# Optimization experiments

Measured on AMD Instinct MI355X. Metric: run time of the kernel, lower is better.

Reference implementation:

```python
import jax, jax.numpy as jnp
import numpy as np

B, T, U = 32, 512, 64
V, H, E = 32000, 512, 512


def setup_inputs() -> dict:
    key = jax.random.key(0)
    ks = jax.random.split(key, 12)
    s = 0.02
    return {
        "encoder_out": jax.random.normal(ks[0], (B, T, E), jnp.float32),
        "encoder_lens": jax.random.randint(ks[1], (B,), 1, T + 1),
        "decoder_in": jax.random.randint(ks[2], (B, U), 0, V),
        "emb_table": jax.random.normal(ks[3], (V, H), jnp.float32) * s,
        "W_attn": jax.random.normal(ks[4], (H, E), jnp.float32) * s,
        "W_ih0": jax.random.normal(ks[5], (3 * H, H + E), jnp.float32) * s,
        "W_hh0": jax.random.normal(ks[6], (3 * H, H), jnp.float32) * s,
        "b_ih0": jnp.zeros((3 * H,), jnp.float32),
        "b_hh0": jnp.zeros((3 * H,), jnp.float32),
        "W_ih1": jax.random.normal(ks[7], (3 * H, H), jnp.float32) * s,
        "W_hh1": jax.random.normal(ks[8], (3 * H, H), jnp.float32) * s,
        "b_ih1": jnp.zeros((3 * H,), jnp.float32),
        "b_hh1": jnp.zeros((3 * H,), jnp.float32),
        "W_out": jax.random.normal(ks[9], (V, H + E), jnp.float32) * s,
        "b_out": jnp.zeros((V,), jnp.float32),
    }


def gru_cell(x, h, W_ih, W_hh, b_ih, b_hh):
    # PyTorch GRUCell gate math
    gi = x @ W_ih.T + b_ih          # [B, 3H]
    gh = h @ W_hh.T + b_hh          # [B, 3H]
    i_r, i_z, i_n = jnp.split(gi, 3, axis=-1)
    h_r, h_z, h_n = jnp.split(gh, 3, axis=-1)
    r = jax.nn.sigmoid(i_r + h_r)
    z = jax.nn.sigmoid(i_z + h_z)
    n = jnp.tanh(i_n + r * h_n)
    return (1.0 - z) * n + z * h


def reference(encoder_out, encoder_lens, decoder_in, emb_table, W_attn,
              W_ih0, W_hh0, b_ih0, b_hh0, W_ih1, W_hh1, b_ih1, b_hh1,
              W_out, b_out):
    b, t_max, e = encoder_out.shape
    u_max = decoder_in.shape[1]
    enc_proj = jnp.einsum('bte,he->bth', encoder_out, W_attn)   # [B,T,H]
    embedded = emb_table[decoder_in]                            # [B,U,H]
    pad_mask = jnp.arange(t_max)[None, :] >= encoder_lens[:, None]  # [B,T]
    h_dim = emb_table.shape[1]

    def step(carry, xs):
        h0, h1 = carry
        emb_t, t = xs                                           # emb_t: [B,H]
        # first step: query is the embedding; afterwards: top-layer hidden
        query = jnp.where(t == 0, emb_t, h1)
        scores = jnp.einsum('bth,bh->bt', enc_proj, query)      # [B,T]
        scores = jnp.where(pad_mask, -jnp.inf, scores)
        attn = jax.nn.softmax(scores, axis=1)
        context = jnp.einsum('bt,bte->be', attn, encoder_out)   # [B,E]
        x = jnp.concatenate([emb_t, context], axis=-1)          # [B,H+E]
        h0n = gru_cell(x, h0, W_ih0, W_hh0, b_ih0, b_hh0)
        h1n = gru_cell(h0n, h1, W_ih1, W_hh1, b_ih1, b_hh1)     # dropout=eval mode (no-op)
        logits = jnp.concatenate([h1n, context], axis=-1) @ W_out.T + b_out  # [B,V]
        return (h0n, h1n), logits

    init = (jnp.zeros((b, h_dim), encoder_out.dtype),
            jnp.zeros((b, h_dim), encoder_out.dtype))
    xs = (jnp.swapaxes(embedded, 0, 1), jnp.arange(u_max))
    _, logits = jax.lax.scan(step, init, xs)                    # [U,B,V]
    return jnp.swapaxes(logits, 0, 1)                           # [B,U,V]
```

## Files before the change

kernel.cpp:

```cpp
#include <hip/hip_runtime.h>
#include <math.h>

#define B_ 32
#define T_ 512
#define U_ 64
#define V_ 32000
#define H_ 512
#define E_ 512

typedef short short8 __attribute__((ext_vector_type(8)));
typedef float f32x4 __attribute__((ext_vector_type(4)));

__global__ void embed_kernel(const int* __restrict__ tok, const float* __restrict__ table,
                             float* __restrict__ out) {
  int row = blockIdx.x;
  int t = tok[row];
  const float4* src = (const float4*)(table + (size_t)t * H_);
  float4* dst = (float4*)(out + (size_t)row * H_);
  dst[threadIdx.x] = src[threadIdx.x];
}

__global__ void zero_kernel(float* p, int n) {
  int i = blockIdx.x * blockDim.x + threadIdx.x;
  if (i < n) p[i] = 0.f;
}

__device__ __forceinline__ unsigned pack1(float f) {
  unsigned u = __float_as_uint(f);
  unsigned hi = u & 0xffff0000u;
  float lo = f - __uint_as_float(hi);
  return hi | (__float_as_uint(lo) >> 16);
}

__global__ __launch_bounds__(256) void pack_kernel(const float4* __restrict__ src,
                                                   uint4* __restrict__ dst, int n4) {
  int i = blockIdx.x * blockDim.x + threadIdx.x;
  if (i < n4) {
    float4 f = src[i];
    uint4 o;
    o.x = pack1(f.x); o.y = pack1(f.y); o.z = pack1(f.z); o.w = pack1(f.w);
    dst[i] = o;
  }
}

__global__ __launch_bounds__(256) void gemm_abt(
    const float* __restrict__ A, const float* __restrict__ Bm,
    const float* __restrict__ bias, float* __restrict__ C,
    int N, int K, int lda, int ldb) {
  __shared__ float As[8][128];
  __shared__ float Bs[8][128];
  int tid = threadIdx.x;
  int n0 = blockIdx.x * 128, m0 = blockIdx.y * 128;
  int lr = tid >> 1;
  int lk = (tid & 1) * 4;
  const float* Ap = A + (size_t)(m0 + lr) * lda + lk;
  const float* Bp = Bm + (size_t)(n0 + lr) * ldb + lk;
  int tx = tid & 15, ty = tid >> 4;
  float acc[8][8];
#pragma unroll
  for (int i = 0; i < 8; i++)
#pragma unroll
    for (int j = 0; j < 8; j++) acc[i][j] = 0.f;

  for (int k0 = 0; k0 < K; k0 += 8) {
    float4 av = *(const float4*)(Ap + k0);
    float4 bv = *(const float4*)(Bp + k0);
    __syncthreads();
    As[lk + 0][lr] = av.x; As[lk + 1][lr] = av.y; As[lk + 2][lr] = av.z; As[lk + 3][lr] = av.w;
    Bs[lk + 0][lr] = bv.x; Bs[lk + 1][lr] = bv.y; Bs[lk + 2][lr] = bv.z; Bs[lk + 3][lr] = bv.w;
    __syncthreads();
#pragma unroll
    for (int kk = 0; kk < 8; kk++) {
      float a[8], b[8];
      *(float4*)&a[0] = *(const float4*)&As[kk][ty * 4];
      *(float4*)&a[4] = *(const float4*)&As[kk][ty * 4 + 64];
      *(float4*)&b[0] = *(const float4*)&Bs[kk][tx * 4];
      *(float4*)&b[4] = *(const float4*)&Bs[kk][tx * 4 + 64];
#pragma unroll
      for (int i = 0; i < 8; i++)
#pragma unroll
        for (int j = 0; j < 8; j++) acc[i][j] = fmaf(a[i], b[j], acc[i][j]);
    }
  }
  float bb[8] = {0, 0, 0, 0, 0, 0, 0, 0};
  if (bias) {
    *(float4*)&bb[0] = *(const float4*)&bias[n0 + tx * 4];
    *(float4*)&bb[4] = *(const float4*)&bias[n0 + tx * 4 + 64];
  }
#pragma unroll
  for (int i = 0; i < 8; i++) {
    int m = m0 + ty * 4 + (i & 3) + (i >> 2) * 64;
    float* Crow = C + (size_t)m * N + n0;
    float4 o0 = make_float4(acc[i][0] + bb[0], acc[i][1] + bb[1], acc[i][2] + bb[2], acc[i][3] + bb[3]);
    float4 o1 = make_float4(acc[i][4] + bb[4], acc[i][5] + bb[5], acc[i][6] + bb[6], acc[i][7] + bb[7]);
    *(float4*)(Crow + tx * 4) = o0;
    *(float4*)(Crow + tx * 4 + 64) = o1;
  }
}

__device__ __forceinline__ void unpack8(uint4 u0, uint4 u1, short8& h, short8& l) {
  h[0] = (short)(u0.x >> 16); l[0] = (short)(u0.x & 0xffffu);
  h[1] = (short)(u0.y >> 16); l[1] = (short)(u0.y & 0xffffu);
  h[2] = (short)(u0.z >> 16); l[2] = (short)(u0.z & 0xffffu);
  h[3] = (short)(u0.w >> 16); l[3] = (short)(u0.w & 0xffffu);
  h[4] = (short)(u1.x >> 16); l[4] = (short)(u1.x & 0xffffu);
  h[5] = (short)(u1.y >> 16); l[5] = (short)(u1.y & 0xffffu);
  h[6] = (short)(u1.z >> 16); l[6] = (short)(u1.z & 0xffffu);
  h[7] = (short)(u1.w >> 16); l[7] = (short)(u1.w & 0xffffu);
}

__global__ __launch_bounds__(256) void gemm_mfma(
    const unsigned* __restrict__ Ap, const unsigned* __restrict__ Bp,
    const float* __restrict__ bias, float* __restrict__ C, int N, int K) {
  __shared__ __align__(16) unsigned As[128 * 64];
  __shared__ __align__(16) unsigned Bs[128 * 64];
  int tid = threadIdx.x;
  int n0 = blockIdx.x * 128, m0 = blockIdx.y * 128;
  int w = tid >> 6, l = tid & 63;
  int wm = (w >> 1) * 64, wn = (w & 1) * 64;
  f32x4 acc[4][4];
#pragma unroll
  for (int i = 0; i < 4; i++)
#pragma unroll
    for (int j = 0; j < 4; j++) acc[i][j] = (f32x4){0.f, 0.f, 0.f, 0.f};

  for (int kt = 0; kt < K; kt += 64) {
    __syncthreads();
#pragma unroll
    for (int i = 0; i < 8; i++) {
      int off16 = tid + i * 256;
      int row = off16 >> 4, c = off16 & 15;
      int sc = c ^ (row & 15);
      *(uint4*)&As[(size_t)off16 * 4] = *(const uint4*)&Ap[(size_t)(m0 + row) * K + kt + sc * 4];
      *(uint4*)&Bs[(size_t)off16 * 4] = *(const uint4*)&Bp[(size_t)(n0 + row) * K + kt + sc * 4];
    }
    __syncthreads();
#pragma unroll
    for (int kk = 0; kk < 2; kk++) {
      short8 ah[4], al[4], bh[4], bl[4];
      int c0 = kk * 8 + (l >> 4) * 2;
#pragma unroll
      for (int fm = 0; fm < 4; fm++) {
        int row = wm + fm * 16 + (l & 15);
        uint4 u0 = *(const uint4*)&As[(row * 16 + (c0 ^ (row & 15))) * 4];
        uint4 u1 = *(const uint4*)&As[(row * 16 + ((c0 + 1) ^ (row & 15))) * 4];
        unpack8(u0, u1, ah[fm], al[fm]);
      }
#pragma unroll
      for (int fn = 0; fn < 4; fn++) {
        int row = wn + fn * 16 + (l & 15);
        uint4 u0 = *(const uint4*)&Bs[(row * 16 + (c0 ^ (row & 15))) * 4];
        uint4 u1 = *(const uint4*)&Bs[(row * 16 + ((c0 + 1) ^ (row & 15))) * 4];
        unpack8(u0, u1, bh[fn], bl[fn]);
      }
#pragma unroll
      for (int fm = 0; fm < 4; fm++)
#pragma unroll
        for (int fn = 0; fn < 4; fn++) {
          acc[fm][fn] = __builtin_amdgcn_mfma_f32_16x16x32_bf16(ah[fm], bh[fn], acc[fm][fn], 0, 0, 0);
          acc[fm][fn] = __builtin_amdgcn_mfma_f32_16x16x32_bf16(ah[fm], bl[fn], acc[fm][fn], 0, 0, 0);
          acc[fm][fn] = __builtin_amdgcn_mfma_f32_16x16x32_bf16(al[fm], bh[fn], acc[fm][fn], 0, 0, 0);
        }
    }
  }
#pragma unroll
  for (int fn = 0; fn < 4; fn++) {
    int n = n0 + wn + fn * 16 + (l & 15);
    float bz = bias ? bias[n] : 0.f;
#pragma unroll
    for (int fm = 0; fm < 4; fm++) {
      int mbase = m0 + wm + fm * 16 + (l >> 4) * 4;
#pragma unroll
      for (int r = 0; r < 4; r++) C[(size_t)(mbase + r) * N + n] = acc[fm][fn][r] + bz;
    }
  }
}

__global__ __launch_bounds__(512) void attn_scores(
    const float* __restrict__ enc_proj, const int* __restrict__ lens,
    const float* __restrict__ embedded, const float* __restrict__ h1_prev,
    float* __restrict__ sc_raw, int u) {
  int s = blockIdx.x, b = blockIdx.y;
  int tid = threadIdx.x;
  __shared__ __align__(16) float q[H_];
  q[tid] = (u == 0) ? embedded[((size_t)b * U_ + u) * H_ + tid] : h1_prev[b * H_ + tid];
  __syncthreads();
  int len = lens[b];
  int w = tid >> 6, l = tid & 63;
  int t0 = s * 64 + w * 8;
  const float4* q4 = (const float4*)q;
  float4 b0 = q4[l], b1 = q4[l + 64];
#pragma unroll
  for (int i = 0; i < 8; i++) {
    int t = t0 + i;
    if (t < len) {
      const float4* r4 = (const float4*)(enc_proj + ((size_t)b * T_ + t) * H_);
      float4 a0 = r4[l], a1 = r4[l + 64];
      float acc = a0.x * b0.x + a0.y * b0.y + a0.z * b0.z + a0.w * b0.w
                + a1.x * b1.x + a1.y * b1.y + a1.z * b1.z + a1.w * b1.w;
#pragma unroll
      for (int off = 32; off > 0; off >>= 1) acc += __shfl_xor(acc, off, 64);
      if (l == 0) sc_raw[b * T_ + t] = acc;
    } else {
      if (l == 0) sc_raw[b * T_ + t] = -INFINITY;
    }
  }
}

__global__ __launch_bounds__(512) void attn_ctx(
    const float* __restrict__ enc_out, const float* __restrict__ sc_raw,
    float* __restrict__ X, int u) {
  int s = blockIdx.x, b = blockIdx.y;
  int tid = threadIdx.x;
  __shared__ float p[T_];
  __shared__ float red[512];
  float v = sc_raw[b * T_ + tid];
  red[tid] = v;
  __syncthreads();
  for (int st = 256; st > 0; st >>= 1) { if (tid < st) red[tid] = fmaxf(red[tid], red[tid + st]); __syncthreads(); }
  float mx = red[0];
  __syncthreads();
  float e = expf(v - mx);
  red[tid] = e;
  __syncthreads();
  for (int st = 256; st > 0; st >>= 1) { if (tid < st) red[tid] += red[tid + st]; __syncthreads(); }
  float inv = 1.f / red[0];
  __syncthreads();
  p[tid] = e * inv;
  __syncthreads();
  int l = tid & 63, stripe = tid >> 6;
  const float* eo = enc_out + (size_t)b * T_ * E_ + s * 64 + l;
  float a0 = 0, a1 = 0, a2 = 0, a3 = 0, a4 = 0, a5 = 0, a6 = 0, a7 = 0;
  for (int t = stripe; t < T_; t += 64) {
    a0 += p[t]      * eo[(size_t)(t)      * E_];
    a1 += p[t +  8] * eo[(size_t)(t +  8) * E_];
    a2 += p[t + 16] * eo[(size_t)(t + 16) * E_];
    a3 += p[t + 24] * eo[(size_t)(t + 24) * E_];
    a4 += p[t + 32] * eo[(size_t)(t + 32) * E_];
    a5 += p[t + 40] * eo[(size_t)(t + 40) * E_];
    a6 += p[t + 48] * eo[(size_t)(t + 48) * E_];
    a7 += p[t + 56] * eo[(size_t)(t + 56) * E_];
  }
  red[tid] = a0 + a1 + a2 + a3 + a4 + a5 + a6 + a7;
  __syncthreads();
  if (tid < 64) {
    float r = red[tid];
#pragma unroll
    for (int i = 1; i < 8; i++) r += red[tid + 64 * i];
    X[((size_t)b * U_ + u) * (H_ + E_) + H_ + s * 64 + tid] = r;
  }
}

__global__ __launch_bounds__(256) void gru0_step(
    const float* __restrict__ X, const float* __restrict__ GI0,
    const float* __restrict__ h_prev, const float* __restrict__ W_ih,
    const float* __restrict__ W_hh, const float* __restrict__ b_ih,
    const float* __restrict__ b_hh, float* __restrict__ h_next, int u) {
  int j = blockIdx.x;
  int tid = threadIdx.x;
  __shared__ __align__(16) float Wr[512], Wz[512], Wn[512], Vr[512], Vz[512], Vn[512];
  __shared__ float red[4][256];
  {
    int h2 = tid & 127;
    const float4* wr4 = (const float4*)(W_ih + (size_t)j * 1024 + 512);
    const float4* wz4 = (const float4*)(W_ih + ((size_t)j + 512) * 1024 + 512);
    const float4* wn4 = (const float4*)(W_ih + ((size_t)j + 1024) * 1024 + 512);
    const float4* vr4 = (const float4*)(W_hh + (size_t)j * 512);
    const float4* vz4 = (const float4*)(W_hh + ((size_t)j + 512) * 512);
    const float4* vn4 = (const float4*)(W_hh + ((size_t)j + 1024) * 512);
    if (tid < 128) {
      ((float4*)Wr)[h2] = wr4[h2];
      ((float4*)Wn)[h2] = wn4[h2];
      ((float4*)Vz)[h2] = vz4[h2];
    } else {
      ((float4*)Wz)[h2] = wz4[h2];
      ((float4*)Vr)[h2] = vr4[h2];
      ((float4*)Vn)[h2] = vn4[h2];
    }
  }
  __syncthreads();
  int b = tid >> 3, s = tid & 7;
  const float4* xc = (const float4*)(X + ((size_t)b * U_ + u) * (H_ + E_) + H_);
  const float4* hp = (const float4*)(h_prev + (size_t)b * H_);
  float ar = 0, az = 0, ain = 0, ahn = 0;
#pragma unroll 4
  for (int i = 0; i < 16; i++) {
    int k4 = s + i * 8;
    float4 xv = xc[k4];
    float4 hv = hp[k4];
    float4 wr = ((const float4*)Wr)[k4];
    float4 wz = ((const float4*)Wz)[k4];
    float4 wn = ((const float4*)Wn)[k4];
    float4 vr = ((const float4*)Vr)[k4];
    float4 vz = ((const float4*)Vz)[k4];
    float4 vn = ((const float4*)Vn)[k4];
    ar += wr.x * xv.x + wr.y * xv.y + wr.z * xv.z + wr.w * xv.w
        + vr.x * hv.x + vr.y * hv.y + vr.z * hv.z + vr.w * hv.w;
    az += wz.x * xv.x + wz.y * xv.y + wz.z * xv.z + wz.w * xv.w
        + vz.x * hv.x + vz.y * hv.y + vz.z * hv.z + vz.w * hv.w;
    ain += wn.x * xv.x + wn.y * xv.y + wn.z * xv.z + wn.w * xv.w;
    ahn += vn.x * hv.x + vn.y * hv.y + vn.z * hv.z + vn.w * hv.w;
  }
  red[0][tid] = ar; red[1][tid] = az; red[2][tid] = ain; red[3][tid] = ahn;
  __syncthreads();
  if (tid < 32) {
    int bb = tid;
    float r = 0, z = 0, in_ = 0, hn = 0;
#pragma unroll
    for (int q2 = 0; q2 < 8; q2++) {
      r += red[0][bb * 8 + q2]; z += red[1][bb * 8 + q2];
      in_ += red[2][bb * 8 + q2]; hn += red[3][bb * 8 + q2];
    }
    size_t grow = ((size_t)bb * U_ + u) * 1536;
    r += GI0[grow + j] + b_ih[j] + b_hh[j];
    z += GI0[grow + 512 + j] + b_ih[512 + j] + b_hh[512 + j];
    in_ += GI0[grow + 1024 + j];
    float rg = 1.f / (1.f + expf(-r));
    float zg = 1.f / (1.f + expf(-z));
    float n = tanhf(in_ + b_ih[1024 + j] + rg * (hn + b_hh[1024 + j]));
    h_next[bb * H_ + j] = (1.f - zg) * n + zg * h_prev[bb * H_ + j];
  }
}

__global__ __launch_bounds__(256) void gru1_step(
    const float* __restrict__ xin, const float* __restrict__ h_prev,
    const float* __restrict__ W_ih, const float* __restrict__ W_hh,
    const float* __restrict__ b_ih, const float* __restrict__ b_hh,
    float* __restrict__ h_next, float* __restrict__ X, int u) {
  int j = blockIdx.x;
  int tid = threadIdx.x;
  __shared__ __align__(16) float Wr[512], Wz[512], Wn[512], Vr[512], Vz[512], Vn[512];
  __shared__ float red[4][256];
  {
    int h2 = tid & 127;
    const float4* wr4 = (const float4*)(W_ih + (size_t)j * 512);
    const float4* wz4 = (const float4*)(W_ih + ((size_t)j + 512) * 512);
    const float4* wn4 = (const float4*)(W_ih + ((size_t)j + 1024) * 512);
    const float4* vr4 = (const float4*)(W_hh + (size_t)j * 512);
    const float4* vz4 = (const float4*)(W_hh + ((size_t)j + 512) * 512);
    const float4* vn4 = (const float4*)(W_hh + ((size_t)j + 1024) * 512);
    if (tid < 128) {
      ((float4*)Wr)[h2] = wr4[h2];
      ((float4*)Wn)[h2] = wn4[h2];
      ((float4*)Vz)[h2] = vz4[h2];
    } else {
      ((float4*)Wz)[h2] = wz4[h2];
      ((float4*)Vr)[h2] = vr4[h2];
      ((float4*)Vn)[h2] = vn4[h2];
    }
  }
  __syncthreads();
  int b = tid >> 3, s = tid & 7;
  const float4* xp = (const float4*)(xin + (size_t)b * H_);
  const float4* hp = (const float4*)(h_prev + (size_t)b * H_);
  float ar = 0, az = 0, ain = 0, ahn = 0;
#pragma unroll 4
  for (int i = 0; i < 16; i++) {
    int k4 = s + i * 8;
    float4 xv = xp[k4];
    float4 hv = hp[k4];
    float4 wr = ((const float4*)Wr)[k4];
    float4 wz = ((const float4*)Wz)[k4];
    float4 wn = ((const float4*)Wn)[k4];
    float4 vr = ((const float4*)Vr)[k4];
    float4 vz = ((const float4*)Vz)[k4];
    float4 vn = ((const float4*)Vn)[k4];
    ar += wr.x * xv.x + wr.y * xv.y + wr.z * xv.z + wr.w * xv.w
        + vr.x * hv.x + vr.y * hv.y + vr.z * hv.z + vr.w * hv.w;
    az += wz.x * xv.x + wz.y * xv.y + wz.z * xv.z + wz.w * xv.w
        + vz.x * hv.x + vz.y * hv.y + vz.z * hv.z + vz.w * hv.w;
    ain += wn.x * xv.x + wn.y * xv.y + wn.z * xv.z + wn.w * xv.w;
    ahn += vn.x * hv.x + vn.y * hv.y + vn.z * hv.z + vn.w * hv.w;
  }
  red[0][tid] = ar; red[1][tid] = az; red[2][tid] = ain; red[3][tid] = ahn;
  __syncthreads();
  if (tid < 32) {
    int bb = tid;
    float r = 0, z = 0, in_ = 0, hn = 0;
#pragma unroll
    for (int q2 = 0; q2 < 8; q2++) {
      r += red[0][bb * 8 + q2]; z += red[1][bb * 8 + q2];
      in_ += red[2][bb * 8 + q2]; hn += red[3][bb * 8 + q2];
    }
    r += b_ih[j] + b_hh[j];
    z += b_ih[512 + j] + b_hh[512 + j];
    float rg = 1.f / (1.f + expf(-r));
    float zg = 1.f / (1.f + expf(-z));
    float n = tanhf(in_ + b_ih[1024 + j] + rg * (hn + b_hh[1024 + j]));
    float ho = (1.f - zg) * n + zg * h_prev[bb * H_ + j];
    h_next[bb * H_ + j] = ho;
    X[((size_t)bb * U_ + u) * (H_ + E_) + j] = ho;
  }
}

extern "C" void kernel_launch(void* const* d_in, const int* in_sizes, int n_in,
                              void* d_out, int out_size, void* d_ws, size_t ws_size,
                              hipStream_t stream) {
  const float* encoder_out  = (const float*)d_in[0];
  const int*   encoder_lens = (const int*)d_in[1];
  const int*   decoder_in   = (const int*)d_in[2];
  const float* emb_table    = (const float*)d_in[3];
  const float* W_attn       = (const float*)d_in[4];
  const float* W_ih0        = (const float*)d_in[5];
  const float* W_hh0        = (const float*)d_in[6];
  const float* b_ih0        = (const float*)d_in[7];
  const float* b_hh0        = (const float*)d_in[8];
  const float* W_ih1        = (const float*)d_in[9];
  const float* W_hh1        = (const float*)d_in[10];
  const float* b_ih1        = (const float*)d_in[11];
  const float* b_hh1        = (const float*)d_in[12];
  const float* W_out        = (const float*)d_in[13];
  const float* b_out        = (const float*)d_in[14];
  float* out = (float*)d_out;

  float* X   = (float*)d_ws;
  float* h0b = X + 2097152;
  float* h1b = h0b + 32768;
  unsigned* Xpack = (unsigned*)(h1b + 32768);
  unsigned* Wpack = Xpack + 2097152;
  size_t ws_need = ((size_t)2097152 + 65536 + 2097152 + 32768000) * 4;
  bool use_mfma = ws_size >= ws_need;

  float* enc_proj = out;
  float* embedded = out + 8388608;
  float* GI0      = out + 9437184;
  float* sc_raw   = out + 12582912;

  zero_kernel<<<256, 256, 0, stream>>>(h0b, 65536);
  embed_kernel<<<B_ * U_, 128, 0, stream>>>(decoder_in, emb_table, embedded);
  gemm_abt<<<dim3(4, 128), 256, 0, stream>>>(encoder_out, W_attn, nullptr, enc_proj, 512, 512, 512, 512);
  gemm_abt<<<dim3(12, 16), 256, 0, stream>>>(embedded, W_ih0, nullptr, GI0, 1536, 512, 512, 1024);
  if (use_mfma) {
    pack_kernel<<<32000, 256, 0, stream>>>((const float4*)W_out, (uint4*)Wpack, 8192000);
  }

  for (int u = 0; u < U_; u++) {
    int cur = u & 1, nxt = cur ^ 1;
    attn_scores<<<dim3(8, B_), 512, 0, stream>>>(enc_proj, encoder_lens, embedded,
                                                 h1b + cur * 16384, sc_raw, u);
    attn_ctx<<<dim3(8, B_), 512, 0, stream>>>(encoder_out, sc_raw, X, u);
    gru0_step<<<512, 256, 0, stream>>>(X, GI0, h0b + cur * 16384, W_ih0, W_hh0,
                                       b_ih0, b_hh0, h0b + nxt * 16384, u);
    gru1_step<<<512, 256, 0, stream>>>(h0b + nxt * 16384, h1b + cur * 16384, W_ih1, W_hh1,
                                       b_ih1, b_hh1, h1b + nxt * 16384, X, u);
  }
  if (use_mfma) {
    pack_kernel<<<2048, 256, 0, stream>>>((const float4*)X, (uint4*)Xpack, 524288);
    gemm_mfma<<<dim3(250, 16), 256, 0, stream>>>(Xpack, Wpack, b_out, out, V_, 1024);
  } else {
    gemm_abt<<<dim3(250, 16), 256, 0, stream>>>(X, W_out, b_out, out, V_, 1024, 1024, 1024);
  }
}
```

Measured before the change: 3.864 ms.

## Fuse decoder recurrence into one persistent cooperative kernel with grid syncs

Replaces the 256 per-step kernel launches of the attention and GRU recurrence with a single cooperative kernel of 256 blocks that loops over all decoder steps, separating phases with grid-wide syncs. Each block keeps its slice of the GRU weights (two hidden units across all gates) resident in shared memory for the whole loop, so those weights are not re-read from global memory every step. The aim is to remove launch overhead and repeated weight traffic. It relies on cooperative launch support and on all 256 blocks being co-resident, and falls back to the old launch loop if the cooperative launch fails.

```diff
diff --git a/kernel.cpp b/kernel.cpp
--- a/kernel.cpp
+++ b/kernel.cpp
@@ -1,5 +1,8 @@
 #include <hip/hip_runtime.h>
+#include <hip/hip_cooperative_groups.h>
 #include <math.h>
+
+namespace cg = cooperative_groups;
 
 #define B_ 32
 #define T_ 512
@@ -173,6 +176,236 @@
 #pragma unroll
       for (int r = 0; r < 4; r++) C[(size_t)(mbase + r) * N + n] = acc[fm][fn][r] + bz;
     }
+  }
+}
+
+__global__ __launch_bounds__(512) void decoder_loop(
+    const float* __restrict__ enc_proj, const float* __restrict__ enc_out,
+    const int* __restrict__ lens, const float* __restrict__ embedded,
+    const float* __restrict__ GI0,
+    float* __restrict__ h0b, float* __restrict__ h1b,
+    float* __restrict__ X, float* __restrict__ sc_raw,
+    const float* __restrict__ W_ih0, const float* __restrict__ W_hh0,
+    const float* __restrict__ b_ih0, const float* __restrict__ b_hh0,
+    const float* __restrict__ W_ih1, const float* __restrict__ W_hh1,
+    const float* __restrict__ b_ih1, const float* __restrict__ b_hh1) {
+  cg::grid_group grid = cg::this_grid();
+  int tid = threadIdx.x;
+  int blk = blockIdx.x;
+  int battn = blk >> 3, sattn = blk & 7;
+  int j0 = blk * 2;
+
+  __shared__ __align__(16) float w0[2][6][512];
+  __shared__ __align__(16) float w1[2][6][512];
+  __shared__ __align__(16) float scr[2048];
+
+  {
+    int e = tid & 127, grp = tid >> 7;
+    int hh = grp >> 1;
+    int j = j0 + hh;
+    if ((grp & 1) == 0) {
+      ((float4*)w0[hh][0])[e] = *((const float4*)(W_ih0 + (size_t)j * 1024 + 512) + e);
+      ((float4*)w0[hh][1])[e] = *((const float4*)(W_ih0 + ((size_t)j + 512) * 1024 + 512) + e);
+      ((float4*)w0[hh][2])[e] = *((const float4*)(W_ih0 + ((size_t)j + 1024) * 1024 + 512) + e);
+      ((float4*)w1[hh][0])[e] = *((const float4*)(W_ih1 + (size_t)j * 512) + e);
+      ((float4*)w1[hh][1])[e] = *((const float4*)(W_ih1 + ((size_t)j + 512) * 512) + e);
+      ((float4*)w1[hh][2])[e] = *((const float4*)(W_ih1 + ((size_t)j + 1024) * 512) + e);
+    } else {
+      ((float4*)w0[hh][3])[e] = *((const float4*)(W_hh0 + (size_t)j * 512) + e);
+      ((float4*)w0[hh][4])[e] = *((const float4*)(W_hh0 + ((size_t)j + 512) * 512) + e);
+      ((float4*)w0[hh][5])[e] = *((const float4*)(W_hh0 + ((size_t)j + 1024) * 512) + e);
+      ((float4*)w1[hh][3])[e] = *((const float4*)(W_hh1 + (size_t)j * 512) + e);
+      ((float4*)w1[hh][4])[e] = *((const float4*)(W_hh1 + ((size_t)j + 512) * 512) + e);
+      ((float4*)w1[hh][5])[e] = *((const float4*)(W_hh1 + ((size_t)j + 1024) * 512) + e);
+    }
+  }
+  __syncthreads();
+  int lenb = lens[battn];
+
+  for (int u = 0; u < U_; u++) {
+    const float* h0_prev = h0b + (u & 1) * 16384;
+    float*       h0_next = h0b + ((u & 1) ^ 1) * 16384;
+    const float* h1_prev = h1b + (u & 1) * 16384;
+    float*       h1_next = h1b + ((u & 1) ^ 1) * 16384;
+
+    {
+      float* q = scr;
+      q[tid] = (u == 0) ? embedded[(size_t)battn * U_ * H_ + tid]
+                        : h1_prev[battn * H_ + tid];
+      __syncthreads();
+      int w = tid >> 6, l = tid & 63;
+      int t0 = sattn * 64 + w * 8;
+      const float4* q4 = (const float4*)q;
+      float4 b0v = q4[l], b1v = q4[l + 64];
+#pragma unroll
+      for (int i = 0; i < 8; i++) {
+        int t = t0 + i;
+        if (t < lenb) {
+          const float4* r4 = (const float4*)(enc_proj + ((size_t)battn * T_ + t) * H_);
+          float4 a0 = r4[l], a1 = r4[l + 64];
+          float acc = a0.x * b0v.x + a0.y * b0v.y + a0.z * b0v.z + a0.w * b0v.w
+                    + a1.x * b1v.x + a1.y * b1v.y + a1.z * b1v.z + a1.w * b1v.w;
+#pragma unroll
+          for (int off = 32; off > 0; off >>= 1) acc += __shfl_xor(acc, off, 64);
+          if (l == 0) sc_raw[battn * T_ + t] = acc;
+        } else {
+          if (l == 0) sc_raw[battn * T_ + t] = -INFINITY;
+        }
+      }
+    }
+    grid.sync();
+
+    {
+      float* red = scr;
+      float* p   = scr + 512;
+      float v = sc_raw[battn * T_ + tid];
+      float m = v;
+#pragma unroll
+      for (int off = 32; off > 0; off >>= 1) m = fmaxf(m, __shfl_xor(m, off, 64));
+      if ((tid & 63) == 0) red[tid >> 6] = m;
+      __syncthreads();
+      float mx = fmaxf(fmaxf(fmaxf(red[0], red[1]), fmaxf(red[2], red[3])),
+                       fmaxf(fmaxf(red[4], red[5]), fmaxf(red[6], red[7])));
+      float ee = expf(v - mx);
+      float sm = ee;
+#pragma unroll
+      for (int off = 32; off > 0; off >>= 1) sm += __shfl_xor(sm, off, 64);
+      if ((tid & 63) == 0) red[8 + (tid >> 6)] = sm;
+      __syncthreads();
+      float tot = ((red[8] + red[9]) + (red[10] + red[11]))
+                + ((red[12] + red[13]) + (red[14] + red[15]));
+      float inv = 1.f / tot;
+      p[tid] = ee * inv;
+      __syncthreads();
+      int l = tid & 63, stripe = tid >> 6;
+      const float* eo = enc_out + (size_t)battn * T_ * E_ + sattn * 64 + l;
+      float a0 = 0, a1 = 0, a2 = 0, a3 = 0, a4 = 0, a5 = 0, a6 = 0, a7 = 0;
+      for (int t = stripe; t < T_; t += 64) {
+        a0 += p[t]      * eo[(size_t)(t)      * E_];
+        a1 += p[t +  8] * eo[(size_t)(t +  8) * E_];
+        a2 += p[t + 16] * eo[(size_t)(t + 16) * E_];
+        a3 += p[t + 24] * eo[(size_t)(t + 24) * E_];
+        a4 += p[t + 32] * eo[(size_t)(t + 32) * E_];
+        a5 += p[t + 40] * eo[(size_t)(t + 40) * E_];
+        a6 += p[t + 48] * eo[(size_t)(t + 48) * E_];
+        a7 += p[t + 56] * eo[(size_t)(t + 56) * E_];
+      }
+      red[tid] = a0 + a1 + a2 + a3 + a4 + a5 + a6 + a7;
+      __syncthreads();
+      if (tid < 64) {
+        float r = red[tid];
+#pragma unroll
+        for (int i = 1; i < 8; i++) r += red[tid + 64 * i];
+        X[((size_t)battn * U_ + u) * (H_ + E_) + H_ + sattn * 64 + tid] = r;
+      }
+    }
+    grid.sync();
+
+    {
+      int half = tid >> 8, t2 = tid & 255;
+      int jj = j0 + half;
+      int b = t2 >> 3, s = t2 & 7;
+      const float4* xc = (const float4*)(X + ((size_t)b * U_ + u) * (H_ + E_) + H_);
+      const float4* hp = (const float4*)(h0_prev + (size_t)b * H_);
+      float ar = 0, az = 0, ain = 0, ahn = 0;
+#pragma unroll 4
+      for (int i = 0; i < 16; i++) {
+        int k4 = s + i * 8;
+        float4 xv = xc[k4];
+        float4 hv = hp[k4];
+        float4 wr = ((const float4*)w0[half][0])[k4];
+        float4 wz = ((const float4*)w0[half][1])[k4];
+        float4 wn = ((const float4*)w0[half][2])[k4];
+        float4 vr = ((const float4*)w0[half][3])[k4];
+        float4 vz = ((const float4*)w0[half][4])[k4];
+        float4 vn = ((const float4*)w0[half][5])[k4];
+        ar += wr.x * xv.x + wr.y * xv.y + wr.z * xv.z + wr.w * xv.w
+            + vr.x * hv.x + vr.y * hv.y + vr.z * hv.z + vr.w * hv.w;
+        az += wz.x * xv.x + wz.y * xv.y + wz.z * xv.z + wz.w * xv.w
+            + vz.x * hv.x + vz.y * hv.y + vz.z * hv.z + vz.w * hv.w;
+        ain += wn.x * xv.x + wn.y * xv.y + wn.z * xv.z + wn.w * xv.w;
+        ahn += vn.x * hv.x + vn.y * hv.y + vn.z * hv.z + vn.w * hv.w;
+      }
+      float* gred = scr;
+      gred[(half * 4 + 0) * 256 + t2] = ar;
+      gred[(half * 4 + 1) * 256 + t2] = az;
+      gred[(half * 4 + 2) * 256 + t2] = ain;
+      gred[(half * 4 + 3) * 256 + t2] = ahn;
+      __syncthreads();
+      if (t2 < 32) {
+        int bb = t2;
+        float r = 0, z = 0, in_ = 0, hn = 0;
+#pragma unroll
+        for (int q2 = 0; q2 < 8; q2++) {
+          r   += gred[(half * 4 + 0) * 256 + bb * 8 + q2];
+          z   += gred[(half * 4 + 1) * 256 + bb * 8 + q2];
+          in_ += gred[(half * 4 + 2) * 256 + bb * 8 + q2];
+          hn  += gred[(half * 4 + 3) * 256 + bb * 8 + q2];
+        }
+        size_t grow = ((size_t)bb * U_ + u) * 1536;
+        r += GI0[grow + jj] + b_ih0[jj] + b_hh0[jj];
+        z += GI0[grow + 512 + jj] + b_ih0[512 + jj] + b_hh0[512 + jj];
+        in_ += GI0[grow + 1024 + jj];
+        float rg = 1.f / (1.f + expf(-r));
+        float zg = 1.f / (1.f + expf(-z));
+        float n = tanhf(in_ + b_ih0[1024 + jj] + rg * (hn + b_hh0[1024 + jj]));
+        h0_next[bb * H_ + jj] = (1.f - zg) * n + zg * h0_prev[bb * H_ + jj];
+      }
+    }
+    grid.sync();
+
+    {
+      int half = tid >> 8, t2 = tid & 255;
+      int jj = j0 + half;
+      int b = t2 >> 3, s = t2 & 7;
+      const float4* xp = (const float4*)(h0_next + (size_t)b * H_);
+      const float4* hp = (const float4*)(h1_prev + (size_t)b * H_);
+      float ar = 0, az = 0, ain = 0, ahn = 0;
+#pragma unroll 4
+      for (int i = 0; i < 16; i++) {
+        int k4 = s + i * 8;
+        float4 xv = xp[k4];
+        float4 hv = hp[k4];
+        float4 wr = ((const float4*)w1[half][0])[k4];
+        float4 wz = ((const float4*)w1[half][1])[k4];
+        float4 wn = ((const float4*)w1[half][2])[k4];
+        float4 vr = ((const float4*)w1[half][3])[k4];
+        float4 vz = ((const float4*)w1[half][4])[k4];
+        float4 vn = ((const float4*)w1[half][5])[k4];
+        ar += wr.x * xv.x + wr.y * xv.y + wr.z * xv.z + wr.w * xv.w
+            + vr.x * hv.x + vr.y * hv.y + vr.z * hv.z + vr.w * hv.w;
+        az += wz.x * xv.x + wz.y * xv.y + wz.z * xv.z + wz.w * xv.w
+            + vz.x * hv.x + vz.y * hv.y + vz.z * hv.z + vz.w * hv.w;
+        ain += wn.x * xv.x + wn.y * xv.y + wn.z * xv.z + wn.w * xv.w;
+        ahn += vn.x * hv.x + vn.y * hv.y + vn.z * hv.z + vn.w * hv.w;
+      }
+      float* gred = scr;
+      gred[(half * 4 + 0) * 256 + t2] = ar;
+      gred[(half * 4 + 1) * 256 + t2] = az;
+      gred[(half * 4 + 2) * 256 + t2] = ain;
+      gred[(half * 4 + 3) * 256 + t2] = ahn;
+      __syncthreads();
+      if (t2 < 32) {
+        int bb = t2;
+        float r = 0, z = 0, in_ = 0, hn = 0;
+#pragma unroll
+        for (int q2 = 0; q2 < 8; q2++) {
+          r   += gred[(half * 4 + 0) * 256 + bb * 8 + q2];
+          z   += gred[(half * 4 + 1) * 256 + bb * 8 + q2];
+          in_ += gred[(half * 4 + 2) * 256 + bb * 8 + q2];
+          hn  += gred[(half * 4 + 3) * 256 + bb * 8 + q2];
+        }
+        r += b_ih1[jj] + b_hh1[jj];
+        z += b_ih1[512 + jj] + b_hh1[512 + jj];
+        float rg = 1.f / (1.f + expf(-r));
+        float zg = 1.f / (1.f + expf(-z));
+        float n = tanhf(in_ + b_ih1[1024 + jj] + rg * (hn + b_hh1[1024 + jj]));
+        float ho = (1.f - zg) * n + zg * h1_prev[bb * H_ + jj];
+        h1_next[bb * H_ + jj] = ho;
+        X[((size_t)bb * U_ + u) * (H_ + E_) + jj] = ho;
+      }
+    }
+    grid.sync();
   }
 }
 
@@ -434,16 +667,35 @@
     pack_kernel<<<32000, 256, 0, stream>>>((const float4*)W_out, (uint4*)Wpack, 8192000);
   }
 
-  for (int u = 0; u < U_; u++) {
-    int cur = u & 1, nxt = cur ^ 1;
-    attn_scores<<<dim3(8, B_), 512, 0, stream>>>(enc_proj, encoder_lens, embedded,
-                                                 h1b + cur * 16384, sc_raw, u);
-    attn_ctx<<<dim3(8, B_), 512, 0, stream>>>(encoder_out, sc_raw, X, u);
-    gru0_step<<<512, 256, 0, stream>>>(X, GI0, h0b + cur * 16384, W_ih0, W_hh0,
-                                       b_ih0, b_hh0, h0b + nxt * 16384, u);
-    gru1_step<<<512, 256, 0, stream>>>(h0b + nxt * 16384, h1b + cur * 16384, W_ih1, W_hh1,
-                                       b_ih1, b_hh1, h1b + nxt * 16384, X, u);
-  }
+  {
+    const float* a_ep = enc_proj; const float* a_eo = encoder_out;
+    const int*   a_ln = encoder_lens; const float* a_em = embedded;
+    const float* a_gi = GI0;
+    float* a_h0 = h0b; float* a_h1 = h1b; float* a_X = X; float* a_sc = sc_raw;
+    const float* a_wi0 = W_ih0; const float* a_wh0 = W_hh0;
+    const float* a_bi0 = b_ih0; const float* a_bh0 = b_hh0;
+    const float* a_wi1 = W_ih1; const float* a_wh1 = W_hh1;
+    const float* a_bi1 = b_ih1; const float* a_bh1 = b_hh1;
+    void* kargs[] = { (void*)&a_ep, (void*)&a_eo, (void*)&a_ln, (void*)&a_em, (void*)&a_gi,
+                      (void*)&a_h0, (void*)&a_h1, (void*)&a_X, (void*)&a_sc,
+                      (void*)&a_wi0, (void*)&a_wh0, (void*)&a_bi0, (void*)&a_bh0,
+                      (void*)&a_wi1, (void*)&a_wh1, (void*)&a_bi1, (void*)&a_bh1 };
+    hipError_t cerr = hipLaunchCooperativeKernel((void*)decoder_loop, dim3(256), dim3(512),
+                                                 kargs, 0, stream);
+    if (cerr != hipSuccess) {
+      for (int u = 0; u < U_; u++) {
+        int cur = u & 1, nxt = cur ^ 1;
+        attn_scores<<<dim3(8, B_), 512, 0, stream>>>(enc_proj, encoder_lens, embedded,
+                                                     h1b + cur * 16384, sc_raw, u);
+        attn_ctx<<<dim3(8, B_), 512, 0, stream>>>(encoder_out, sc_raw, X, u);
+        gru0_step<<<512, 256, 0, stream>>>(X, GI0, h0b + cur * 16384, W_ih0, W_hh0,
+                                           b_ih0, b_hh0, h0b + nxt * 16384, u);
+        gru1_step<<<512, 256, 0, stream>>>(h0b + nxt * 16384, h1b + cur * 16384, W_ih1, W_hh1,
+                                           b_ih1, b_hh1, h1b + nxt * 16384, X, u);
+      }
+    }
+  }
+
   if (use_mfma) {
     pack_kernel<<<2048, 256, 0, stream>>>((const float4*)X, (uint4*)Xpack, 524288);
     gemm_mfma<<<dim3(250, 16), 256, 0, stream>>>(Xpack, Wpack, b_out, out, V_, 1024);
```

After: 10.85 ms. 2.81x slower.
